# Optimization experiments

Hardware: AMD Instinct MI355X
Metric: run time of the kernel (lower is better)

## Reference

```python
import jax, jax.numpy as jnp
import numpy as np

B, N, D, H = 64, 196, 768, 3072
QMAX = 127.0  # 8-bit symmetric: clamp to [-128, 127]


def ste_round(x):
    # straight-through-estimator round (QAT)
    return x + jax.lax.stop_gradient(jnp.round(x) - x)


def q_linear_diag(x, w, b, a_sf):
    """Quantized diagonal linear (ResMLP Affine / LayerScale as QuantLinear)."""
    w_sf = jnp.max(jnp.abs(w)) / QMAX            # per-tensor weight scale
    w_int = ste_round(w / w_sf)                  # int8 weights (|.|<=127)
    out_int = (x / a_sf) * w_int
    if b is not None:
        out_int = out_int + ste_round(b / (a_sf * w_sf))  # 32-bit bias
    return out_int * (a_sf * w_sf), w_sf


def q_linear_dense(x, w, b, a_sf):
    """Quantized dense linear: int8 GEMM + int32 bias, dequant with a_sf*w_sf."""
    w_sf = jnp.max(jnp.abs(w)) / QMAX
    w_int = jnp.clip(ste_round(w / w_sf), -QMAX - 1, QMAX)
    out_int = jnp.einsum('...i,oi->...o', x / a_sf, w_int) + ste_round(b / (a_sf * w_sf))
    return out_int * (a_sf * w_sf), w_sf


def q_act(x, pre_sf, new_sf, identity=None, id_sf=None):
    """HAWQ-style QuantAct: fixed-point requantization to scale new_sf (8-bit)."""
    if identity is None:
        z_int = ste_round(x / pre_sf)
        out_int = ste_round(z_int * (pre_sf / new_sf))
    else:
        # main branch (x - identity) requantized with pre_sf, identity with id_sf
        z_int = ste_round((x - identity) / pre_sf)
        out_int = ste_round(z_int * (pre_sf / new_sf)) \
                + ste_round(ste_round(identity / id_sf) * (id_sf / new_sf))
    out_int = jnp.clip(out_int, -QMAX - 1, QMAX)
    return out_int * new_sf, new_sf


def _forward(x, norm1_w, norm1_b, attn_w, attn_b, gamma1_w,
             norm2_w, norm2_b, fc1_w, fc1_b, fc2_w, fc2_b, gamma2_w, act_sfs):
    a_sf = act_sfs[0]
    # --- token-mixing half ---
    identity, id_sf = x, a_sf
    x, w_sf = q_linear_diag(x, norm1_w, norm1_b, a_sf)         # norm1 (affine)
    x = jnp.swapaxes(x, 1, 2)                                  # [B, D, N]
    x, a_sf = q_act(x, a_sf * w_sf, act_sfs[1])                # quant_act1
    x, w_sf = q_linear_dense(x, attn_w, attn_b, a_sf)          # attn (cross-patch)
    x = jnp.swapaxes(x, 1, 2)                                  # [B, N, D]
    x, a_sf = q_act(x, a_sf * w_sf, act_sfs[2])                # quant_act2
    x, w_sf = q_linear_diag(x, gamma1_w, None, a_sf)           # gamma_1 (layerscale)
    x = x + identity
    x, a_sf = q_act(x, a_sf * w_sf, act_sfs[3], identity, id_sf)  # quant_act_int32_1
    # --- MLP half ---
    identity, id_sf = x, a_sf
    x, w_sf = q_linear_diag(x, norm2_w, norm2_b, a_sf)         # norm2
    x, a_sf = q_act(x, a_sf * w_sf, act_sfs[4])                # quant_act3
    x, w_sf = q_linear_dense(x, fc1_w, fc1_b, a_sf)            # mlp.fc1
    x = jax.nn.relu(x)
    x, a_sf = q_act(x, a_sf * w_sf, act_sfs[5])                # mlp.quant_act1
    x, w_sf = q_linear_dense(x, fc2_w, fc2_b, a_sf)            # mlp.fc2
    x, a_sf = q_act(x, a_sf * w_sf, act_sfs[6])                # mlp.quant_act2
    x, w_sf = q_linear_diag(x, gamma2_w, None, a_sf)           # gamma_2
    x = x + identity
    x, a_sf = q_act(x, a_sf * w_sf, act_sfs[7], identity, id_sf)  # quant_act_int32_2
    return x, a_sf


def setup_inputs() -> dict:
    key = jax.random.key(0)
    ks = jax.random.split(key, 16)
    act_sfs = jax.random.uniform(ks[14], (8,), jnp.float32, 0.02, 0.06)
    x = jax.random.normal(ks[0], (B, N, D), jnp.float32)
    # input is already quantized at scale act_sfs[0]
    x = jnp.clip(jnp.round(x / act_sfs[0]), -128, 127) * act_sfs[0]
    s = 0.05
    return {
        'x': x,
        'norm1_w': 1.0 + s * jax.random.normal(ks[1], (D,), jnp.float32),
        'norm1_b': s * jax.random.normal(ks[2], (D,), jnp.float32),
        'attn_w': jax.random.normal(ks[3], (N, N), jnp.float32) / np.sqrt(N),
        'attn_b': s * jax.random.normal(ks[4], (N,), jnp.float32),
        'gamma1_w': 0.1 + s * jax.random.normal(ks[5], (D,), jnp.float32),
        'norm2_w': 1.0 + s * jax.random.normal(ks[6], (D,), jnp.float32),
        'norm2_b': s * jax.random.normal(ks[7], (D,), jnp.float32),
        'fc1_w': jax.random.normal(ks[8], (H, D), jnp.float32) / np.sqrt(D),
        'fc1_b': s * jax.random.normal(ks[9], (H,), jnp.float32),
        'fc2_w': jax.random.normal(ks[10], (D, H), jnp.float32) / np.sqrt(H),
        'fc2_b': s * jax.random.normal(ks[11], (D,), jnp.float32),
        'gamma2_w': 0.1 + s * jax.random.normal(ks[12], (D,), jnp.float32),
        'act_sfs': act_sfs,
    }


def reference(x, norm1_w, norm1_b, attn_w, attn_b, gamma1_w,
              norm2_w, norm2_b, fc1_w, fc1_b, fc2_w, fc2_b, gamma2_w, act_sfs):
    return _forward(x, norm1_w, norm1_b, attn_w, attn_b, gamma1_w,
                    norm2_w, norm2_b, fc1_w, fc1_b, fc2_w, fc2_b, gamma2_w, act_sfs)
```

## Files before the change

kernel.cpp:

```cpp
#include <hip/hip_runtime.h>

#define B_ 64
#define N_ 196
#define D_ 768
#define H_ 3072
#define M_ (B_*N_)
#define NP 256

typedef int int4v __attribute__((ext_vector_type(4)));
typedef signed char i8;

#define WS_MAX 0
#define WS_W1F 16
#define WS_B1F (16+768)
#define WS_G1F (16+768*2)
#define WS_W2F (16+768*3)
#define WS_B2F (16+768*4)
#define WS_G2F (16+768*5)
#define WS_BA  (16+768*6)
#define WS_BF1 (WS_BA+256)
#define WS_BF2 (WS_BF1+3072)
#define OFF_WA   40960ull
#define OFF_FC1  (OFF_WA+65536ull)
#define OFF_FC2  (OFF_FC1+2359296ull)
#define OFF_X2   (OFF_FC2+2359296ull)
#define OFF_Q3   (OFF_X2+9633792ull)
#define OFF_Q4   (OFF_Q3+9633792ull)
#define OFF_Q1T  OFF_Q4
#define OFF_X8   (OFF_Q4+12582912ull)

__device__ __forceinline__ float clamp8(float v){ return fminf(fmaxf(v,-128.f),127.f); }

__device__ __forceinline__ void async16(const void* g, void* l){
    __builtin_amdgcn_global_load_lds((const __attribute__((address_space(1))) void*)g,
                                     (__attribute__((address_space(3))) void*)l, 16, 0, 0);
}

__global__ void k_init(char* ws, const float* __restrict__ act, float* out_tail){
    int id = blockIdx.x*256 + threadIdx.x;
    if (blockIdx.x == 0){
        float* f = (float*)ws;
        if (threadIdx.x < 8) f[WS_MAX+threadIdx.x] = 0.f;
        if (threadIdx.x == 8) *out_tail = act[7];
    }
    if (id < 4096){ int4v z = {0,0,0,0}; ((int4v*)(ws+OFF_WA))[id] = z; }
}

__global__ void k_maxabs(const float* __restrict__ p0, const float* __restrict__ p1,
                         const float* __restrict__ p2, const float* __restrict__ p3,
                         const float* __restrict__ p4, const float* __restrict__ p5,
                         const float* __restrict__ p6, float* wsmax){
    const float* ps[7] = {p0,p1,p2,p3,p4,p5,p6};
    const int    n4s[7] = {192, 9604, 192, 192, 589824, 589824, 192};
    int tid = blockIdx.y;
    const float4* p = (const float4*)ps[tid]; int n4 = n4s[tid];
    float m = 0.f;
    for (int i = blockIdx.x*blockDim.x + threadIdx.x; i < n4; i += gridDim.x*blockDim.x){
        float4 v = p[i];
        m = fmaxf(m, fmaxf(fmaxf(fabsf(v.x),fabsf(v.y)), fmaxf(fabsf(v.z),fabsf(v.w))));
    }
    #pragma unroll
    for (int off = 32; off; off >>= 1) m = fmaxf(m, __shfl_down(m, off, 64));
    __shared__ float red[4];
    int lane = threadIdx.x & 63, wv = threadIdx.x >> 6;
    if (lane == 0) red[wv] = m;
    __syncthreads();
    if (threadIdx.x == 0){
        float mm = red[0];
        for (int w = 1; w < (int)blockDim.x/64; w++) mm = fmaxf(mm, red[w]);
        atomicMax((unsigned*)&wsmax[tid], __float_as_uint(mm));
    }
}

__global__ void k_qweights(const float* __restrict__ n1w, const float* __restrict__ n1b,
                           const float* __restrict__ aw,  const float* __restrict__ ab,
                           const float* __restrict__ g1w, const float* __restrict__ n2w,
                           const float* __restrict__ n2b, const float* __restrict__ f1w,
                           const float* __restrict__ f1b, const float* __restrict__ f2w,
                           const float* __restrict__ f2b, const float* __restrict__ g2w,
                           const float* __restrict__ act, char* ws){
    float* fws = (float*)ws;
    int*   iws = (int*)ws;
    const float* mx = fws + WS_MAX;
    long i = (long)blockIdx.x*blockDim.x + threadIdx.x;
    const long F4 = 589824;
    if (i < F4){ float sf = mx[4]/127.0f;
        float4 v = ((const float4*)f1w)[i];
        char4 o = make_char4(
            (i8)(int)fminf(fmaxf(rintf(v.x/sf),-128.f),127.f),
            (i8)(int)fminf(fmaxf(rintf(v.y/sf),-128.f),127.f),
            (i8)(int)fminf(fmaxf(rintf(v.z/sf),-128.f),127.f),
            (i8)(int)fminf(fmaxf(rintf(v.w/sf),-128.f),127.f));
        ((char4*)(ws+OFF_FC1))[i] = o; return; }
    i -= F4;
    if (i < F4){ float sf = mx[5]/127.0f;
        float4 v = ((const float4*)f2w)[i];
        char4 o = make_char4(
            (i8)(int)fminf(fmaxf(rintf(v.x/sf),-128.f),127.f),
            (i8)(int)fminf(fmaxf(rintf(v.y/sf),-128.f),127.f),
            (i8)(int)fminf(fmaxf(rintf(v.z/sf),-128.f),127.f),
            (i8)(int)fminf(fmaxf(rintf(v.w/sf),-128.f),127.f));
        ((char4*)(ws+OFF_FC2))[i] = o; return; }
    i -= F4;
    if (i < 38416){ float sf = mx[1]/127.0f;
        int o = (int)(i/196), k = (int)(i%196);
        ((i8*)(ws+OFF_WA))[o*NP+k] = (i8)(int)fminf(fmaxf(rintf(aw[i]/sf),-128.f),127.f); return; }
    i -= 38416;
    if (i < 768){ float sf = mx[0]/127.0f; fws[WS_W1F+i] = rintf(n1w[i]/sf); return; }
    i -= 768;
    if (i < 768){ float sf = mx[0]/127.0f; fws[WS_B1F+i] = rintf(n1b[i]/(act[0]*sf)); return; }
    i -= 768;
    if (i < 768){ float sf = mx[2]/127.0f; fws[WS_G1F+i] = rintf(g1w[i]/sf); return; }
    i -= 768;
    if (i < 768){ float sf = mx[3]/127.0f; fws[WS_W2F+i] = rintf(n2w[i]/sf); return; }
    i -= 768;
    if (i < 768){ float sf = mx[3]/127.0f; fws[WS_B2F+i] = rintf(n2b[i]/(act[3]*sf)); return; }
    i -= 768;
    if (i < 768){ float sf = mx[6]/127.0f; fws[WS_G2F+i] = rintf(g2w[i]/sf); return; }
    i -= 768;
    if (i < 196){ float sf = mx[1]/127.0f; iws[WS_BA+i] = (int)rintf(ab[i]/(act[1]*sf)); return; }
    i -= 196;
    if (i < 3072){ float sf = mx[4]/127.0f; iws[WS_BF1+i] = (int)rintf(f1b[i]/(act[4]*sf)); return; }
    i -= 3072;
    if (i < 768){ float sf = mx[5]/127.0f; iws[WS_BF2+i] = (int)rintf(f2b[i]/(act[5]*sf)); return; }
}

__global__ __launch_bounds__(256) void k_stage1(const float* __restrict__ x,
                                                const char* __restrict__ wsc,
                                                char* __restrict__ ws,
                                                const float* __restrict__ act){
    __shared__ i8 T[64][68];
    const float* fws = (const float*)wsc;
    int b = blockIdx.z, n0 = blockIdx.y*64, d0 = blockIdx.x*64;
    int t = threadIdx.x;
    float a0 = act[0];
    float w1sf = fws[WS_MAX+0]/127.0f;
    float r1 = (a0*w1sf)/act[1];
    int dl = (t & 15) * 4;
    int d  = d0 + dl;
    float4 wv = *(const float4*)(fws + WS_W1F + d);
    float4 bv = *(const float4*)(fws + WS_B1F + d);
    i8* x8 = (i8*)(ws + OFF_X8);
    #pragma unroll
    for (int pass = 0; pass < 4; pass++){
        int nl = (t >> 4) + pass*16;
        int n  = n0 + nl;
        i8 q[4] = {0,0,0,0};
        if (n < 196){
            float4 xv = *(const float4*)(x + ((size_t)b*196 + n)*768 + d);
            float i0 = rintf(xv.x/a0), i1 = rintf(xv.y/a0);
            float i2 = rintf(xv.z/a0), i3 = rintf(xv.w/a0);
            *(char4*)(x8 + ((size_t)b*196 + n)*768 + d) =
                make_char4((i8)(int)i0,(i8)(int)i1,(i8)(int)i2,(i8)(int)i3);
            float o0 = rintf(i0*wv.x + bv.x);
            float o1 = rintf(i1*wv.y + bv.y);
            float o2 = rintf(i2*wv.z + bv.z);
            float o3 = rintf(i3*wv.w + bv.w);
            q[0] = (i8)(int)clamp8(rintf(o0*r1));
            q[1] = (i8)(int)clamp8(rintf(o1*r1));
            q[2] = (i8)(int)clamp8(rintf(o2*r1));
            q[3] = (i8)(int)clamp8(rintf(o3*r1));
        }
        T[dl+0][nl] = q[0]; T[dl+1][nl] = q[1];
        T[dl+2][nl] = q[2]; T[dl+3][nl] = q[3];
    }
    __syncthreads();
    i8* q1T = (i8*)(ws + OFF_Q1T) + (size_t)b*768*NP;
    #pragma unroll
    for (int e = 0; e < 4; e++){
        int id = t + e*256;
        int row = id >> 4, c = (id & 15) * 4;
        int v = *(const int*)&T[row][c];
        *(int*)(q1T + (size_t)(d0+row)*NP + n0 + c) = v;
    }
}

__device__ __forceinline__ void gemm_i8_dbuf(const i8* __restrict__ qa, const i8* __restrict__ wb,
                                             size_t lda, size_t ldb,
                                             int m0, int n0, int K, int4v acc[4][4],
                                             i8* As, i8* Bs, int t){
    int lane = t & 63;
    int w = t >> 6;
    int wm = w & 1, wn = w >> 1;
    int lr = lane >> 2, lc = lane & 3;
    const i8* ga = qa + (size_t)(m0 + w*32 + lr)*lda + lc*16;
    const i8* gb = wb + (size_t)(n0 + w*32 + lr)*ldb + lc*16;
    int loff = (w*32 + lr)*64 + lc*16;
    async16(ga,            As + loff);
    async16(ga + 16*lda,   As + loff + 16*64);
    async16(gb,            Bs + loff);
    async16(gb + 16*ldb,   Bs + loff + 16*64);
    int iters = K >> 6;
    for (int i = 0; i < iters; i++){
        __syncthreads();
        if (i+1 < iters){
            int kb = (i+1) << 6;
            int nb = ((i+1)&1) << 13;
            async16(ga + kb,            As + nb + loff);
            async16(ga + kb + 16*lda,   As + nb + loff + 16*64);
            async16(gb + kb,            Bs + nb + loff);
            async16(gb + kb + 16*ldb,   Bs + nb + loff + 16*64);
        }
        int cb = (i&1) << 13;
        int4v a[4], bb[4];
        #pragma unroll
        for (int mt = 0; mt < 4; mt++)
            a[mt] = *(const int4v*)(As + cb + (wm*64+mt*16+(lane&15))*64 + (lane>>4)*16);
        #pragma unroll
        for (int nt = 0; nt < 4; nt++)
            bb[nt] = *(const int4v*)(Bs + cb + (wn*64+nt*16+(lane&15))*64 + (lane>>4)*16);
        #pragma unroll
        for (int mt = 0; mt < 4; mt++)
            #pragma unroll
            for (int nt = 0; nt < 4; nt++)
                acc[mt][nt] = __builtin_amdgcn_mfma_i32_16x16x64_i8(a[mt], bb[nt], acc[mt][nt], 0,0,0);
    }
}

__device__ __forceinline__ void gemm_i8_512(const i8* __restrict__ qa, const i8* __restrict__ wb,
                                            size_t lda, size_t ldb,
                                            int m0, int n0, int K, int4v acc[4][2],
                                            i8* As, i8* Bs, int t){
    int lane = t & 63;
    int w = t >> 6;
    int wm = w & 1, wn = w >> 1;
    int sr = t >> 2, sc = t & 3;
    const i8* ga = qa + (size_t)(m0 + sr)*lda + sc*16;
    const i8* gb = wb + (size_t)(n0 + sr)*ldb + sc*16;
    int loff = sr*64 + sc*16;
    async16(ga, As + loff);
    async16(gb, Bs + loff);
    int arow = (wm*64 + (lane&15))*64 + (lane>>4)*16;
    int brow = (wn*32 + (lane&15))*64 + (lane>>4)*16;
    int iters = K >> 6;
    for (int i = 0; i < iters; i++){
        __syncthreads();
        if (i+1 < iters){
            int kb = (i+1) << 6;
            int nb = ((i+1)&1) << 13;
            async16(ga + kb, As + nb + loff);
            async16(gb + kb, Bs + nb + loff);
        }
        int cb = (i&1) << 13;
        int4v a[4], bb[2];
        #pragma unroll
        for (int mt = 0; mt < 4; mt++)
            a[mt] = *(const int4v*)(As + cb + arow + mt*16*64);
        #pragma unroll
        for (int nt = 0; nt < 2; nt++)
            bb[nt] = *(const int4v*)(Bs + cb + brow + nt*16*64);
        #pragma unroll
        for (int mt = 0; mt < 4; mt++)
            #pragma unroll
            for (int nt = 0; nt < 2; nt++)
                acc[mt][nt] = __builtin_amdgcn_mfma_i32_16x16x64_i8(a[mt], bb[nt], acc[mt][nt], 0,0,0);
    }
}

__global__ __launch_bounds__(256) void k_attn(const char* __restrict__ ws,
                                              const float* __restrict__ act){
    __shared__ char smem[32768];
    const float* fws = (const float*)ws;
    const int*   iws = (const int*)ws;
    const i8* A  = (const i8*)(ws + OFF_WA);
    const i8* Bq = (const i8*)(ws + OFF_Q1T) + (size_t)blockIdx.z*768*NP;
    const i8* x8 = (const i8*)(ws + OFF_X8);
    i8* x2 = (i8*)(ws + OFF_X2);
    i8* q3 = (i8*)(ws + OFF_Q3);
    int b = blockIdx.z;
    int m0 = blockIdx.x*128, n0 = blockIdx.y*128;
    int t = threadIdx.x, lane = t & 63;
    int wm = (t>>6)&1, wn = t>>7;
    int4v acc[4][4]; int4v zz = {0,0,0,0};
    #pragma unroll
    for (int mt=0;mt<4;mt++) for (int nt=0;nt<4;nt++) acc[mt][nt] = zz;
    gemm_i8_dbuf(A, Bq, NP, NP, m0, n0, NP, acc, (i8*)smem, (i8*)smem+16384, t);

    float a1=act[1], a2=act[2], a3=act[3], a4=act[4];
    float wasf = fws[WS_MAX+1]/127.0f; float r2  = (a1*wasf)/a2;
    float g1sf = fws[WS_MAX+2]/127.0f; float r3a = (a2*g1sf)/a3; float r3b = act[0]/a3;
    float w2sf = fws[WS_MAX+3]/127.0f; float r4  = (a3*w2sf)/a4;
    float g1v[4], w2v[4], b2v[4];
    #pragma unroll
    for (int nt=0;nt<4;nt++){
        int d = n0 + wn*64 + nt*16 + (lane&15);
        g1v[nt] = fws[WS_G1F + d]; w2v[nt] = fws[WS_W2F + d]; b2v[nt] = fws[WS_B2F + d];
    }
    __syncthreads();
    i8* Xs = (i8*)smem;
    i8* Qs = (i8*)smem + 16384;
    #pragma unroll
    for (int mt=0;mt<4;mt++){
        #pragma unroll
        for (int r=0;r<4;r++){
            int ml = wm*64 + mt*16 + (lane>>4)*4 + r;
            int o  = m0 + ml;
            int ba = iws[WS_BA + o];
            #pragma unroll
            for (int nt=0;nt<4;nt++){
                int nl = wn*64 + nt*16 + (lane&15);
                int d  = n0 + nl;
                float s2 = (float)(acc[mt][nt][r] + ba);
                float q2 = clamp8(rintf(s2*r2));
                float o3v = q2*g1v[nt];
                float idi = (o < 196) ? (float)x8[((size_t)b*196 + o)*768 + d] : 0.f;
                float tt = rintf(o3v*r3a) + rintf(idi*r3b);
                tt = clamp8(tt);
                float o4 = tt*w2v[nt] + b2v[nt];
                float qr = clamp8(rintf(o4*r4));
                Xs[ml*128 + nl] = (i8)(int)tt;
                Qs[ml*128 + nl] = (i8)(int)qr;
            }
        }
    }
    __syncthreads();
    #pragma unroll
    for (int e=0;e<4;e++){
        int id = t + e*256;
        int row = id>>3, c = id&7;
        int o = m0 + row;
        if (o < 196){
            size_t g = ((size_t)b*196 + o)*768 + n0 + c*16;
            *(int4v*)(x2 + g) = *(const int4v*)(Xs + row*128 + c*16);
            *(int4v*)(q3 + g) = *(const int4v*)(Qs + row*128 + c*16);
        }
    }
}

__global__ __launch_bounds__(512) void k_fc1(const char* __restrict__ ws, const float* __restrict__ act){
    __shared__ char smem[32768];
    const float* fws = (const float*)ws;
    const int*   iws = (const int*)ws;
    const i8* qa = (const i8*)(ws+OFF_Q3);
    const i8* wb = (const i8*)(ws+OFF_FC1);
    const int* bias = iws + WS_BF1;
    i8* qout = (i8*)(ws+OFF_Q4);
    int m0 = blockIdx.x*128, n0 = blockIdx.y*128;
    int t = threadIdx.x, lane = t & 63;
    int w = t >> 6, wm = w & 1, wn = w >> 1;
    int4v acc[4][2]; int4v zz = {0,0,0,0};
    #pragma unroll
    for (int mt=0;mt<4;mt++) for (int nt=0;nt<2;nt++) acc[mt][nt] = zz;
    gemm_i8_512(qa, wb, 768, 768, m0, n0, 768, acc, (i8*)smem, (i8*)smem+16384, t);
    float wsf = fws[WS_MAX+4]/127.0f;
    float r5 = (act[4]*wsf)/act[5];
    int bcol[2];
    #pragma unroll
    for (int nt=0;nt<2;nt++) bcol[nt] = bias[n0 + wn*32 + nt*16 + (lane&15)];
    __syncthreads();
    i8* Cs = (i8*)smem;
    #pragma unroll
    for (int mt=0;mt<4;mt++){
        #pragma unroll
        for (int nt=0;nt<2;nt++){
            int nl = wn*32 + nt*16 + (lane&15);
            #pragma unroll
            for (int r=0;r<4;r++){
                int s = acc[mt][nt][r] + bcol[nt];
                if (s < 0) s = 0;
                float q = clamp8(rintf((float)s * r5));
                int ml = wm*64 + mt*16 + (lane>>4)*4 + r;
                Cs[ml*128 + nl] = (i8)(int)q;
            }
        }
    }
    __syncthreads();
    #pragma unroll
    for (int e=0;e<2;e++){
        int id2 = t + e*512;
        int row = id2>>3, c = id2&7;
        *(int4v*)(qout + (size_t)(m0+row)*3072 + n0 + c*16) = *(const int4v*)(Cs + row*128 + c*16);
    }
}

__global__ __launch_bounds__(512) void k_fc2(const char* __restrict__ ws, const float* __restrict__ act,
                                             float* __restrict__ out){
    __shared__ char smem[32768];
    const float* fws = (const float*)ws;
    const int*   iws = (const int*)ws;
    const i8* qa = (const i8*)(ws+OFF_Q4);
    const i8* wb = (const i8*)(ws+OFF_FC2);
    const int* bias = iws + WS_BF2;
    const float* g2f = fws + WS_G2F;
    const i8* x2 = (const i8*)(ws+OFF_X2);
    int m0 = blockIdx.x*128, n0 = blockIdx.y*128;
    int t = threadIdx.x, lane = t & 63;
    int w = t >> 6, wm = w & 1, wn = w >> 1;
    int4v acc[4][2]; int4v zz = {0,0,0,0};
    #pragma unroll
    for (int mt=0;mt<4;mt++) for (int nt=0;nt<2;nt++) acc[mt][nt] = zz;
    gemm_i8_512(qa, wb, 3072, 3072, m0, n0, 3072, acc, (i8*)smem, (i8*)smem+16384, t);
    float a3=act[3], a5=act[5], a6=act[6], a7=act[7];
    float wsf  = fws[WS_MAX+5]/127.0f; float r6  = (a5*wsf)/a6;
    float g2sf = fws[WS_MAX+6]/127.0f; float r7a = (a6*g2sf)/a7; float r7b = a3/a7;
    int bcol[2]; float g2v[2];
    #pragma unroll
    for (int nt=0;nt<2;nt++){
        int nc = n0 + wn*32 + nt*16 + (lane&15);
        bcol[nt] = bias[nc]; g2v[nt] = g2f[nc];
    }
    #pragma unroll
    for (int mt=0;mt<4;mt++){
        #pragma unroll
        for (int nt=0;nt<2;nt++){
            int nc = n0 + wn*32 + nt*16 + (lane&15);
            #pragma unroll
            for (int r=0;r<4;r++){
                int ml = wm*64 + mt*16 + (lane>>4)*4 + r;
                size_t gi = (size_t)(m0+ml)*768 + nc;
                int s = acc[mt][nt][r] + bcol[nt];
                float q6 = clamp8(rintf((float)s*r6));
                float o7 = q6*g2v[nt];
                float idi = (float)x2[gi];
                float tt = rintf(o7*r7a) + rintf(idi*r7b);
                tt = clamp8(tt);
                out[gi] = tt*a7;
            }
        }
    }
}

extern "C" void kernel_launch(void* const* d_in, const int* in_sizes, int n_in,
                              void* d_out, int out_size, void* d_ws, size_t ws_size,
                              hipStream_t stream){
    const float* x   = (const float*)d_in[0];
    const float* n1w = (const float*)d_in[1];
    const float* n1b = (const float*)d_in[2];
    const float* aw  = (const float*)d_in[3];
    const float* ab  = (const float*)d_in[4];
    const float* g1w = (const float*)d_in[5];
    const float* n2w = (const float*)d_in[6];
    const float* n2b = (const float*)d_in[7];
    const float* f1w = (const float*)d_in[8];
    const float* f1b = (const float*)d_in[9];
    const float* f2w = (const float*)d_in[10];
    const float* f2b = (const float*)d_in[11];
    const float* g2w = (const float*)d_in[12];
    const float* act = (const float*)d_in[13];
    char* ws = (char*)d_ws;
    float* out = (float*)d_out;

    k_init<<<16,256,0,stream>>>(ws, act, out + (size_t)B_*N_*D_);
    k_maxabs<<<dim3(120,7),256,0,stream>>>(n1w, aw, g1w, n2w, f1w, f2w, g2w, (float*)ws);
    long qwThreads = 2L*589824 + 38416 + 768L*6 + 196 + 3072 + 768;
    k_qweights<<<(int)((qwThreads+255)/256),256,0,stream>>>(n1w,n1b,aw,ab,g1w,n2w,n2b,
                                                            f1w,f1b,f2w,f2b,g2w,act,ws);
    k_stage1<<<dim3(12,4,64),256,0,stream>>>(x, ws, ws, act);
    k_attn<<<dim3(2,6,64),256,0,stream>>>(ws, act);
    k_fc1<<<dim3(98,24),512,0,stream>>>(ws, act);
    k_fc2<<<dim3(98,6),512,0,stream>>>(ws, act, out);
}
```

Before: 272.6 us.

## Store int8 GEMM operands in pre-tiled blocked layout for contiguous tile loads

Quantized weights and intermediate activations (q1T, q3, q4, attn/fc1/fc2 weights) are now written in a blocked 128-row x 64-k tile layout, with 16-byte k-chunks stored column-major inside each tile. Each GEMM K-step then loads one contiguous 8KB tile per operand and can read it straight into LDS with no bank-conflict-prone row striding. The aim is to cut strided global accesses and LDS bank conflicts in all three GEMMs. The cost is scattered writes in the producer epilogues and the weight quantizer, and more complex index arithmetic.

```diff
diff --git a/kernel.cpp b/kernel.cpp
--- a/kernel.cpp
+++ b/kernel.cpp
@@ -72,6 +72,10 @@
     }
 }
 
+__device__ __forceinline__ size_t cm_off(int o, int k, int KC){
+    return (((size_t)(o>>7)*KC + (k>>6))<<13) + (((k>>4)&3)<<11) + ((o&127)<<4) + (k&15);
+}
+
 __global__ void k_qweights(const float* __restrict__ n1w, const float* __restrict__ n1b,
                            const float* __restrict__ aw,  const float* __restrict__ ab,
                            const float* __restrict__ g1w, const float* __restrict__ n2w,
@@ -86,25 +90,28 @@
     const long F4 = 589824;
     if (i < F4){ float sf = mx[4]/127.0f;
         float4 v = ((const float4*)f1w)[i];
-        char4 o = make_char4(
-            (i8)(int)fminf(fmaxf(rintf(v.x/sf),-128.f),127.f),
-            (i8)(int)fminf(fmaxf(rintf(v.y/sf),-128.f),127.f),
-            (i8)(int)fminf(fmaxf(rintf(v.z/sf),-128.f),127.f),
-            (i8)(int)fminf(fmaxf(rintf(v.w/sf),-128.f),127.f));
-        ((char4*)(ws+OFF_FC1))[i] = o; return; }
+        int o = (int)(i/192), kb = (int)(i%192)*4;
+        unsigned b0 = (unsigned)(unsigned char)(i8)(int)fminf(fmaxf(rintf(v.x/sf),-128.f),127.f);
+        unsigned b1 = (unsigned)(unsigned char)(i8)(int)fminf(fmaxf(rintf(v.y/sf),-128.f),127.f);
+        unsigned b2 = (unsigned)(unsigned char)(i8)(int)fminf(fmaxf(rintf(v.z/sf),-128.f),127.f);
+        unsigned b3 = (unsigned)(unsigned char)(i8)(int)fminf(fmaxf(rintf(v.w/sf),-128.f),127.f);
+        *(unsigned*)(ws + OFF_FC1 + cm_off(o, kb, 12)) = b0 | (b1<<8) | (b2<<16) | (b3<<24);
+        return; }
     i -= F4;
     if (i < F4){ float sf = mx[5]/127.0f;
         float4 v = ((const float4*)f2w)[i];
-        char4 o = make_char4(
-            (i8)(int)fminf(fmaxf(rintf(v.x/sf),-128.f),127.f),
-            (i8)(int)fminf(fmaxf(rintf(v.y/sf),-128.f),127.f),
-            (i8)(int)fminf(fmaxf(rintf(v.z/sf),-128.f),127.f),
-            (i8)(int)fminf(fmaxf(rintf(v.w/sf),-128.f),127.f));
-        ((char4*)(ws+OFF_FC2))[i] = o; return; }
+        int o = (int)(i/768), kb = (int)(i%768)*4;
+        unsigned b0 = (unsigned)(unsigned char)(i8)(int)fminf(fmaxf(rintf(v.x/sf),-128.f),127.f);
+        unsigned b1 = (unsigned)(unsigned char)(i8)(int)fminf(fmaxf(rintf(v.y/sf),-128.f),127.f);
+        unsigned b2 = (unsigned)(unsigned char)(i8)(int)fminf(fmaxf(rintf(v.z/sf),-128.f),127.f);
+        unsigned b3 = (unsigned)(unsigned char)(i8)(int)fminf(fmaxf(rintf(v.w/sf),-128.f),127.f);
+        *(unsigned*)(ws + OFF_FC2 + cm_off(o, kb, 48)) = b0 | (b1<<8) | (b2<<16) | (b3<<24);
+        return; }
     i -= F4;
     if (i < 38416){ float sf = mx[1]/127.0f;
         int o = (int)(i/196), k = (int)(i%196);
-        ((i8*)(ws+OFF_WA))[o*NP+k] = (i8)(int)fminf(fmaxf(rintf(aw[i]/sf),-128.f),127.f); return; }
+        ((i8*)(ws+OFF_WA))[cm_off(o, k, 4)] =
+            (i8)(int)fminf(fmaxf(rintf(aw[i]/sf),-128.f),127.f); return; }
     i -= 38416;
     if (i < 768){ float sf = mx[0]/127.0f; fws[WS_W1F+i] = rintf(n1w[i]/sf); return; }
     i -= 768;
@@ -165,94 +172,85 @@
         T[dl+2][nl] = q[2]; T[dl+3][nl] = q[3];
     }
     __syncthreads();
-    i8* q1T = (i8*)(ws + OFF_Q1T) + (size_t)b*768*NP;
+    i8* q1T = (i8*)(ws + OFF_Q1T) + (size_t)b*196608;
     #pragma unroll
     for (int e = 0; e < 4; e++){
         int id = t + e*256;
         int row = id >> 4, c = (id & 15) * 4;
+        int dd = d0 + row;
         int v = *(const int*)&T[row][c];
-        *(int*)(q1T + (size_t)(d0+row)*NP + n0 + c) = v;
-    }
-}
-
-__device__ __forceinline__ void gemm_i8_dbuf(const i8* __restrict__ qa, const i8* __restrict__ wb,
-                                             size_t lda, size_t ldb,
-                                             int m0, int n0, int K, int4v acc[4][4],
-                                             i8* As, i8* Bs, int t){
+        size_t dst = (((size_t)(dd>>7)*4 + blockIdx.y)<<13) + ((size_t)(c>>4)<<11)
+                     + ((dd&127)<<4) + (c&15);
+        *(int*)(q1T + dst) = v;
+    }
+}
+
+__device__ __forceinline__ void gemm_cm_512(const i8* __restrict__ gA, const i8* __restrict__ gB,
+                                            int iters, int4v acc[4][2], i8* As, i8* Bs, int t){
     int lane = t & 63;
-    int w = t >> 6;
-    int wm = w & 1, wn = w >> 1;
-    int lr = lane >> 2, lc = lane & 3;
-    const i8* ga = qa + (size_t)(m0 + w*32 + lr)*lda + lc*16;
-    const i8* gb = wb + (size_t)(n0 + w*32 + lr)*ldb + lc*16;
-    int loff = (w*32 + lr)*64 + lc*16;
-    async16(ga,            As + loff);
-    async16(ga + 16*lda,   As + loff + 16*64);
-    async16(gb,            Bs + loff);
-    async16(gb + 16*ldb,   Bs + loff + 16*64);
-    int iters = K >> 6;
+    int w = t >> 6, wm = w & 1, wn = w >> 1;
+    int lo = t*16;
+    async16(gA + lo, As + lo);
+    async16(gB + lo, Bs + lo);
+    int arow = (lane>>4)*2048 + (wm*64 + (lane&15))*16;
+    int brow = (lane>>4)*2048 + (wn*32 + (lane&15))*16;
     for (int i = 0; i < iters; i++){
         __syncthreads();
         if (i+1 < iters){
-            int kb = (i+1) << 6;
             int nb = ((i+1)&1) << 13;
-            async16(ga + kb,            As + nb + loff);
-            async16(ga + kb + 16*lda,   As + nb + loff + 16*64);
-            async16(gb + kb,            Bs + nb + loff);
-            async16(gb + kb + 16*ldb,   Bs + nb + loff + 16*64);
+            size_t kb = (size_t)(i+1) << 13;
+            async16(gA + kb + lo, As + nb + lo);
+            async16(gB + kb + lo, Bs + nb + lo);
+        }
+        int cb = (i&1) << 13;
+        int4v a[4], bb[2];
+        #pragma unroll
+        for (int mt = 0; mt < 4; mt++)
+            a[mt] = *(const int4v*)(As + cb + arow + mt*256);
+        #pragma unroll
+        for (int nt = 0; nt < 2; nt++)
+            bb[nt] = *(const int4v*)(Bs + cb + brow + nt*256);
+        #pragma unroll
+        for (int mt = 0; mt < 4; mt++)
+            #pragma unroll
+            for (int nt = 0; nt < 2; nt++)
+                acc[mt][nt] = __builtin_amdgcn_mfma_i32_16x16x64_i8(a[mt], bb[nt], acc[mt][nt], 0,0,0);
+    }
+}
+
+__device__ __forceinline__ void gemm_cm_256(const i8* __restrict__ gA, const i8* __restrict__ gB,
+                                            int iters, int4v acc[4][4], i8* As, i8* Bs, int t){
+    int lane = t & 63;
+    int wm = (t>>6)&1, wn = t>>7;
+    int lo = t*16;
+    async16(gA + lo,        As + lo);
+    async16(gA + 4096 + lo, As + 4096 + lo);
+    async16(gB + lo,        Bs + lo);
+    async16(gB + 4096 + lo, Bs + 4096 + lo);
+    int arow = (lane>>4)*2048 + (wm*64 + (lane&15))*16;
+    int brow = (lane>>4)*2048 + (wn*64 + (lane&15))*16;
+    for (int i = 0; i < iters; i++){
+        __syncthreads();
+        if (i+1 < iters){
+            int nb = ((i+1)&1) << 13;
+            size_t kb = (size_t)(i+1) << 13;
+            async16(gA + kb + lo,        As + nb + lo);
+            async16(gA + kb + 4096 + lo, As + nb + 4096 + lo);
+            async16(gB + kb + lo,        Bs + nb + lo);
+            async16(gB + kb + 4096 + lo, Bs + nb + 4096 + lo);
         }
         int cb = (i&1) << 13;
         int4v a[4], bb[4];
         #pragma unroll
         for (int mt = 0; mt < 4; mt++)
-            a[mt] = *(const int4v*)(As + cb + (wm*64+mt*16+(lane&15))*64 + (lane>>4)*16);
+            a[mt] = *(const int4v*)(As + cb + arow + mt*256);
         #pragma unroll
         for (int nt = 0; nt < 4; nt++)
-            bb[nt] = *(const int4v*)(Bs + cb + (wn*64+nt*16+(lane&15))*64 + (lane>>4)*16);
+            bb[nt] = *(const int4v*)(Bs + cb + brow + nt*256);
         #pragma unroll
         for (int mt = 0; mt < 4; mt++)
             #pragma unroll
             for (int nt = 0; nt < 4; nt++)
-                acc[mt][nt] = __builtin_amdgcn_mfma_i32_16x16x64_i8(a[mt], bb[nt], acc[mt][nt], 0,0,0);
-    }
-}
-
-__device__ __forceinline__ void gemm_i8_512(const i8* __restrict__ qa, const i8* __restrict__ wb,
-                                            size_t lda, size_t ldb,
-                                            int m0, int n0, int K, int4v acc[4][2],
-                                            i8* As, i8* Bs, int t){
-    int lane = t & 63;
-    int w = t >> 6;
-    int wm = w & 1, wn = w >> 1;
-    int sr = t >> 2, sc = t & 3;
-    const i8* ga = qa + (size_t)(m0 + sr)*lda + sc*16;
-    const i8* gb = wb + (size_t)(n0 + sr)*ldb + sc*16;
-    int loff = sr*64 + sc*16;
-    async16(ga, As + loff);
-    async16(gb, Bs + loff);
-    int arow = (wm*64 + (lane&15))*64 + (lane>>4)*16;
-    int brow = (wn*32 + (lane&15))*64 + (lane>>4)*16;
-    int iters = K >> 6;
-    for (int i = 0; i < iters; i++){
-        __syncthreads();
-        if (i+1 < iters){
-            int kb = (i+1) << 6;
-            int nb = ((i+1)&1) << 13;
-            async16(ga + kb, As + nb + loff);
-            async16(gb + kb, Bs + nb + loff);
-        }
-        int cb = (i&1) << 13;
-        int4v a[4], bb[2];
-        #pragma unroll
-        for (int mt = 0; mt < 4; mt++)
-            a[mt] = *(const int4v*)(As + cb + arow + mt*16*64);
-        #pragma unroll
-        for (int nt = 0; nt < 2; nt++)
-            bb[nt] = *(const int4v*)(Bs + cb + brow + nt*16*64);
-        #pragma unroll
-        for (int mt = 0; mt < 4; mt++)
-            #pragma unroll
-            for (int nt = 0; nt < 2; nt++)
                 acc[mt][nt] = __builtin_amdgcn_mfma_i32_16x16x64_i8(a[mt], bb[nt], acc[mt][nt], 0,0,0);
     }
 }
@@ -262,19 +260,19 @@
     __shared__ char smem[32768];
     const float* fws = (const float*)ws;
     const int*   iws = (const int*)ws;
-    const i8* A  = (const i8*)(ws + OFF_WA);
-    const i8* Bq = (const i8*)(ws + OFF_Q1T) + (size_t)blockIdx.z*768*NP;
-    const i8* x8 = (const i8*)(ws + OFF_X8);
-    i8* x2 = (i8*)(ws + OFF_X2);
-    i8* q3 = (i8*)(ws + OFF_Q3);
     int b = blockIdx.z;
     int m0 = blockIdx.x*128, n0 = blockIdx.y*128;
+    const i8* gA = (const i8*)(ws + OFF_WA)  + ((size_t)(m0>>7))*32768;
+    const i8* gB = (const i8*)(ws + OFF_Q1T) + (size_t)b*196608 + ((size_t)(n0>>7))*32768;
+    const i8* x8 = (const i8*)(ws + OFF_X8);
+    i8* x2  = (i8*)(ws + OFF_X2);
+    i8* q3  = (i8*)(ws + OFF_Q3);
     int t = threadIdx.x, lane = t & 63;
     int wm = (t>>6)&1, wn = t>>7;
     int4v acc[4][4]; int4v zz = {0,0,0,0};
     #pragma unroll
     for (int mt=0;mt<4;mt++) for (int nt=0;nt<4;nt++) acc[mt][nt] = zz;
-    gemm_i8_dbuf(A, Bq, NP, NP, m0, n0, NP, acc, (i8*)smem, (i8*)smem+16384, t);
+    gemm_cm_256(gA, gB, 4, acc, (i8*)smem, (i8*)smem+16384, t);
 
     float a1=act[1], a2=act[2], a3=act[3], a4=act[4];
     float wasf = fws[WS_MAX+1]/127.0f; float r2  = (a1*wasf)/a2;
@@ -320,9 +318,12 @@
         int row = id>>3, c = id&7;
         int o = m0 + row;
         if (o < 196){
-            size_t g = ((size_t)b*196 + o)*768 + n0 + c*16;
+            int rg = b*196 + o;
+            size_t g = (size_t)rg*768 + n0 + c*16;
             *(int4v*)(x2 + g) = *(const int4v*)(Xs + row*128 + c*16);
-            *(int4v*)(q3 + g) = *(const int4v*)(Qs + row*128 + c*16);
+            size_t dst = (((size_t)(rg>>7)*12 + (n0>>6) + (c>>2))<<13)
+                         + ((size_t)(c&3)<<11) + ((rg&127)<<4);
+            *(int4v*)(q3 + dst) = *(const int4v*)(Qs + row*128 + c*16);
         }
     }
 }
@@ -331,17 +332,17 @@
     __shared__ char smem[32768];
     const float* fws = (const float*)ws;
     const int*   iws = (const int*)ws;
-    const i8* qa = (const i8*)(ws+OFF_Q3);
-    const i8* wb = (const i8*)(ws+OFF_FC1);
+    int m0 = blockIdx.x*128, n0 = blockIdx.y*128;
+    const i8* gA = (const i8*)(ws+OFF_Q3)  + ((size_t)blockIdx.x)*12*8192;
+    const i8* gB = (const i8*)(ws+OFF_FC1) + ((size_t)blockIdx.y)*12*8192;
     const int* bias = iws + WS_BF1;
-    i8* qout = (i8*)(ws+OFF_Q4);
-    int m0 = blockIdx.x*128, n0 = blockIdx.y*128;
+    i8* q4 = (i8*)(ws+OFF_Q4);
     int t = threadIdx.x, lane = t & 63;
     int w = t >> 6, wm = w & 1, wn = w >> 1;
     int4v acc[4][2]; int4v zz = {0,0,0,0};
     #pragma unroll
     for (int mt=0;mt<4;mt++) for (int nt=0;nt<2;nt++) acc[mt][nt] = zz;
-    gemm_i8_512(qa, wb, 768, 768, m0, n0, 768, acc, (i8*)smem, (i8*)smem+16384, t);
+    gemm_cm_512(gA, gB, 12, acc, (i8*)smem, (i8*)smem+16384, t);
     float wsf = fws[WS_MAX+4]/127.0f;
     float r5 = (act[4]*wsf)/act[5];
     int bcol[2];
@@ -367,9 +368,11 @@
     __syncthreads();
     #pragma unroll
     for (int e=0;e<2;e++){
-        int id2 = t + e*512;
-        int row = id2>>3, c = id2&7;
-        *(int4v*)(qout + (size_t)(m0+row)*3072 + n0 + c*16) = *(const int4v*)(Cs + row*128 + c*16);
+        int id = t + e*512;
+        int row = id>>3, c = id&7;
+        size_t dst = (((size_t)blockIdx.x*48 + (n0>>6) + (c>>2))<<13)
+                     + ((size_t)(c&3)<<11) + ((size_t)row<<4);
+        *(int4v*)(q4 + dst) = *(const int4v*)(Cs + row*128 + c*16);
     }
 }
 
@@ -378,18 +381,18 @@
     __shared__ char smem[32768];
     const float* fws = (const float*)ws;
     const int*   iws = (const int*)ws;
-    const i8* qa = (const i8*)(ws+OFF_Q4);
-    const i8* wb = (const i8*)(ws+OFF_FC2);
+    int m0 = blockIdx.x*128, n0 = blockIdx.y*128;
+    const i8* gA = (const i8*)(ws+OFF_Q4)  + ((size_t)blockIdx.x)*48*8192;
+    const i8* gB = (const i8*)(ws+OFF_FC2) + ((size_t)blockIdx.y)*48*8192;
     const int* bias = iws + WS_BF2;
     const float* g2f = fws + WS_G2F;
     const i8* x2 = (const i8*)(ws+OFF_X2);
-    int m0 = blockIdx.x*128, n0 = blockIdx.y*128;
     int t = threadIdx.x, lane = t & 63;
     int w = t >> 6, wm = w & 1, wn = w >> 1;
     int4v acc[4][2]; int4v zz = {0,0,0,0};
     #pragma unroll
     for (int mt=0;mt<4;mt++) for (int nt=0;nt<2;nt++) acc[mt][nt] = zz;
-    gemm_i8_512(qa, wb, 3072, 3072, m0, n0, 3072, acc, (i8*)smem, (i8*)smem+16384, t);
+    gemm_cm_512(gA, gB, 48, acc, (i8*)smem, (i8*)smem+16384, t);
     float a3=act[3], a5=act[5], a6=act[6], a7=act[7];
     float wsf  = fws[WS_MAX+5]/127.0f; float r6  = (a5*wsf)/a6;
     float g2sf = fws[WS_MAX+6]/127.0f; float r7a = (a6*g2sf)/a7; float r7b = a3/a7;
```

Measured after the change: 261.9 us. -3.9%, faster.
